# Kernel tuning notes

Hardware: AMD Instinct MI355X
Metric: run time of the kernel (lower is better)

Reference implementation:

```python
import jax, jax.numpy as jnp
import numpy as np

N, C, NUM_SPECIES, D = 2048, 128, 10, 9  # nodes, channels, species, irreps dim (0e+1o+2e)
IR_DIMS = {"0e": 1, "1o": 3, "2e": 5}
MULS = {3: {"0e": 10, "1o": 11, "2e": 13}, 2: {"0e": 3, "1o": 2, "2e": 3}, 1: {"0e": 1, "1o": 1, "2e": 1}}
IRS = ("0e", "1o", "2e")


def setup_inputs() -> dict:
    key = jax.random.key(0)
    ks = iter(jax.random.split(key, 64))
    inp = {}
    inp["node_feats"] = jax.random.normal(next(ks), (N, C, D), dtype=jnp.float32)
    inp["index"] = jax.random.randint(next(ks), (N,), 0, NUM_SPECIES)
    for order in (3, 2, 1):
        for ir in IRS:
            mul, irdim = MULS[order][ir], IR_DIMS[ir]
            u = jax.random.normal(next(ks), (D,) * order + (mul, irdim), dtype=jnp.float32) * 0.1
            mask = jax.random.bernoulli(next(ks), 0.2, u.shape).astype(jnp.float32)
            inp[f"U{order}_{ir}"] = u * mask
            # learnable per-species weights, stddev mul**-0.5 (gradient_normalization='element')
            inp[f"W{order}_{ir}"] = jax.random.normal(next(ks), (NUM_SPECIES, mul, C), dtype=jnp.float32) * (mul ** -0.5)
    return inp


def _forward(x, index, Us, Ws):
    # x: [N, C, D] node features; index: [N] species ids
    out = {}
    for order in (3, 2, 1):
        created = set()
        for ir in IRS:
            u = Us[(order, ir)]                 # (D,)*order + (mul, ir_dim)
            w = Ws[(order, ir)][index]          # [N, mul, C] species-indexed gather
            if ir not in out:
                # first appearance: contract one feature index j and the basis mul k at once
                out[ir] = jnp.einsum('...jki,nkc,ncj->nc...i', u, w, x)
                created.add(ir)
            else:
                out[ir] = out[ir] + jnp.einsum('...ki,nkc->nc...i', u, w)
        for ir in IRS:
            if ir in created:
                continue
            # contract one remaining feature index with x each order
            out[ir] = jnp.einsum('nc...ji,ncj->nc...i', out[ir], x)
    # concat chunks in sorted irreps order (0e, 1o, 2e) -> [N, C, 9]
    return jnp.concatenate([out[ir] for ir in IRS], axis=-1)


def reference(node_feats, index, U3_0e, U3_1o, U3_2e, U2_0e, U2_1o, U2_2e, U1_0e, U1_1o, U1_2e,
              W3_0e, W3_1o, W3_2e, W2_0e, W2_1o, W2_2e, W1_0e, W1_1o, W1_2e):
    Us = {(3, '0e'): U3_0e, (3, '1o'): U3_1o, (3, '2e'): U3_2e,
          (2, '0e'): U2_0e, (2, '1o'): U2_1o, (2, '2e'): U2_2e,
          (1, '0e'): U1_0e, (1, '1o'): U1_1o, (1, '2e'): U1_2e}
    Ws = {(3, '0e'): W3_0e, (3, '1o'): W3_1o, (3, '2e'): W3_2e,
          (2, '0e'): W2_0e, (2, '1o'): W2_1o, (2, '2e'): W2_2e,
          (1, '0e'): W1_0e, (1, '1o'): W1_1o, (1, '2e'): W1_2e}
    return _forward(node_feats, index, Us, Ws)
```

## Files before the change

kernel.cpp:

```cpp
#include <hip/hip_runtime.h>

#define N_NODES 2048
#define C_CH    128
#define N_SPEC  10

#define PAGE2   2048
#define NMONO   219
#define MAIN_F  1752

#define US3_0   0
#define US3_1   1650
#define US3_2   7095
#define US2_0   17820
#define US2_1   17955
#define US2_2   18225
#define US_TOT  18900

#define US_OFF_B  (128 * 1024)
#define CG_OFF_B  (256 * 1024)
#define CG_BYTES  ((size_t)N_SPEC * C_CH * PAGE2 * 4)

__global__ __launch_bounds__(1024) void bucket_kernel(const int* __restrict__ index,
                                                      int* __restrict__ counts,
                                                      int* __restrict__ lists) {
    __shared__ int sc[N_SPEC];
    const int tid = threadIdx.x;
    if (tid < N_SPEC) sc[tid] = 0;
    __syncthreads();
    for (int n = tid; n < N_NODES; n += blockDim.x) {
        int s = index[n];
        int pos = atomicAdd(&sc[s], 1);
        lists[s * N_NODES + pos] = n;
    }
    __syncthreads();
    if (tid < N_SPEC) counts[tid] = sc[tid];
}

struct Params {
    const float* U3[3]; const float* W3[3];
    const float* U2[3]; const float* W2[3];
    const float* U1[3]; const float* W1[3];
};

__global__ __launch_bounds__(256) void usym_kernel(Params p, float* __restrict__ Us) {
    const int t = blockIdx.x * 256 + threadIdx.x;
    if (t >= US_TOT) return;

    bool is3; int mul, ird, r; const float* u;
    if (t < US3_1)       { is3 = true;  mul = 10; ird = 1; r = t;          u = p.U3[0]; }
    else if (t < US3_2)  { is3 = true;  mul = 11; ird = 3; r = t - US3_1;  u = p.U3[1]; }
    else if (t < US2_0)  { is3 = true;  mul = 13; ird = 5; r = t - US3_2;  u = p.U3[2]; }
    else if (t < US2_1)  { is3 = false; mul = 3;  ird = 1; r = t - US2_0;  u = p.U2[0]; }
    else if (t < US2_2)  { is3 = false; mul = 2;  ird = 3; r = t - US2_1;  u = p.U2[1]; }
    else                 { is3 = false; mul = 3;  ird = 5; r = t - US2_2;  u = p.U2[2]; }

    const int mi  = mul * ird;
    const int n   = r / mi;
    const int rem = r - n * mi;

    float acc = 0.f;
    if (is3) {
        int aa = 0, bb = 0, jj = 0, ctr = 0;
        for (int a2 = 0; a2 < 9; ++a2)
            for (int b2 = a2; b2 < 9; ++b2)
                for (int j2 = b2; j2 < 9; ++j2) {
                    if (ctr == n) { aa = a2; bb = b2; jj = j2; }
                    ++ctr;
                }
        int L[6];
        L[0] = (aa * 9 + bb) * 9 + jj; L[1] = (aa * 9 + jj) * 9 + bb;
        L[2] = (bb * 9 + aa) * 9 + jj; L[3] = (bb * 9 + jj) * 9 + aa;
        L[4] = (jj * 9 + aa) * 9 + bb; L[5] = (jj * 9 + bb) * 9 + aa;
        for (int m = 0; m < 6; ++m) {
            bool dup = false;
            for (int mm = 0; mm < m; ++mm) dup = dup || (L[mm] == L[m]);
            if (!dup) acc += u[L[m] * mi + rem];
        }
    } else {
        int aa = 0, bb = 0, ctr = 0;
        for (int a2 = 0; a2 < 9; ++a2)
            for (int b2 = a2; b2 < 9; ++b2) {
                if (ctr == n) { aa = a2; bb = b2; }
                ++ctr;
            }
        acc = u[(aa * 9 + bb) * mi + rem];
        if (aa != bb) acc += u[(bb * 9 + aa) * mi + rem];
    }
    Us[t] = acc;
}

template <int MUL, int IRD, int IOFF, int MOFF>
__device__ inline void coefRegion(const float* __restrict__ src,
                                  const float* __restrict__ W,
                                  int s, int row0, int rows,
                                  float* __restrict__ Cg, float* __restrict__ sU) {
    const int c   = threadIdx.x;
    float wv[MUL];
#pragma unroll
    for (int k = 0; k < MUL; ++k) wv[k] = W[(s * MUL + k) * C_CH + c];

    const int nfl = rows * MUL * IRD;
    const float* sp = src + row0 * MUL * IRD;
    for (int f = c; f < nfl; f += 128) sU[f] = sp[f];
    __syncthreads();

    const size_t pb = (size_t)(s * C_CH + c) * PAGE2;
    for (int rr = 0; rr < rows; ++rr) {
        const int m = MOFF + row0 + rr;
#pragma unroll
        for (int il = 0; il < IRD; ++il) {
            float a = 0.f;
#pragma unroll
            for (int k = 0; k < MUL; ++k)
                a += sU[(rr * MUL + k) * IRD + il] * wv[k];
            const int i = IOFF + il;
            Cg[pb + (i < 8 ? m * 8 + i : MAIN_F + m)] = a;
        }
    }
}

__global__ __launch_bounds__(128) void coef_kernel(Params p, const float* __restrict__ Us,
                                                   float* __restrict__ Cg) {
    __shared__ float sU[1560];
    const int s = blockIdx.x / 30;
    const int t = blockIdx.x % 30;

    if (t < 7) {
        int rel = t, row0 = rel * 24, rows = (rel == 6) ? 21 : 24;
        coefRegion<10, 1, 0, 0>(Us + US3_0, p.W3[0], s, row0, rows, Cg, sU);
    } else if (t < 14) {
        int rel = t - 7, row0 = rel * 24, rows = (rel == 6) ? 21 : 24;
        coefRegion<11, 3, 1, 0>(Us + US3_1, p.W3[1], s, row0, rows, Cg, sU);
    } else if (t < 21) {
        int rel = t - 14, row0 = rel * 24, rows = (rel == 6) ? 21 : 24;
        coefRegion<13, 5, 4, 0>(Us + US3_2, p.W3[2], s, row0, rows, Cg, sU);
    } else if (t < 23) {
        int rel = t - 21, row0 = rel * 24, rows = (rel == 1) ? 21 : 24;
        coefRegion<3, 1, 0, 165>(Us + US2_0, p.W2[0], s, row0, rows, Cg, sU);
    } else if (t < 25) {
        int rel = t - 23, row0 = rel * 24, rows = (rel == 1) ? 21 : 24;
        coefRegion<2, 3, 1, 165>(Us + US2_1, p.W2[1], s, row0, rows, Cg, sU);
    } else if (t < 27) {
        int rel = t - 25, row0 = rel * 24, rows = (rel == 1) ? 21 : 24;
        coefRegion<3, 5, 4, 165>(Us + US2_2, p.W2[2], s, row0, rows, Cg, sU);
    } else if (t == 27) {
        coefRegion<1, 1, 0, 210>(p.U1[0], p.W1[0], s, 0, 9, Cg, sU);
    } else if (t == 28) {
        coefRegion<1, 3, 1, 210>(p.U1[1], p.W1[1], s, 0, 9, Cg, sU);
    } else {
        coefRegion<1, 5, 4, 210>(p.U1[2], p.W1[2], s, 0, 9, Cg, sU);
    }
}

__device__ inline float selx(const float x[9], int a) {
    float r = x[0];
    r = (a == 1) ? x[1] : r; r = (a == 2) ? x[2] : r; r = (a == 3) ? x[3] : r;
    r = (a == 4) ? x[4] : r; r = (a == 5) ? x[5] : r; r = (a == 6) ? x[6] : r;
    r = (a == 7) ? x[7] : r; r = (a == 8) ? x[8] : r;
    return r;
}

__global__ __launch_bounds__(128) void sc_eval_kernel(const float* __restrict__ nf,
                                                      const int* __restrict__ counts,
                                                      const int* __restrict__ lists,
                                                      const float* __restrict__ Cg,
                                                      float* __restrict__ out) {
    __shared__ __align__(16) float sP[PAGE2];
    const int s = blockIdx.x / C_CH;
    const int c = blockIdx.x % C_CH;
    const float* __restrict__ Cp = Cg + (size_t)(s * C_CH + c) * PAGE2;

    {
        const float4* g = (const float4*)Cp;
        float4* l = (float4*)sP;
#pragma unroll
        for (int q = 0; q < 4; ++q) l[threadIdx.x + 128 * q] = g[threadIdx.x + 128 * q];
    }
    __syncthreads();

    const int cnt = counts[s];
    const float4* __restrict__ Cv = (const float4*)sP;
    const float*  __restrict__ Ct = sP + MAIN_F;

    for (int base = 0; base < cnt; base += 256) {
        const int i0 = base + threadIdx.x;
        const int i1 = base + 128 + threadIdx.x;
        const int m0 = (i0 < cnt) ? lists[s * N_NODES + i0] : -1;
        const int m1 = (i1 < cnt) ? lists[s * N_NODES + i1] : -1;

        const float* x0p = nf + ((long)(m0 < 0 ? 0 : m0) * C_CH + c) * 9;
        const float* x1p = nf + ((long)(m1 < 0 ? 0 : m1) * C_CH + c) * 9;
        float x0[9], x1[9];
#pragma unroll
        for (int j = 0; j < 9; ++j) { x0[j] = x0p[j]; x1[j] = x1p[j]; }

        float4 o0a = {0, 0, 0, 0}, o0b = {0, 0, 0, 0};
        float4 o1a = {0, 0, 0, 0}, o1b = {0, 0, 0, 0};
        float o08 = 0.f, o18 = 0.f;

        const float4* p3 = Cv;
        const float*  t3 = Ct;
        const float4* p2 = Cv + 165 * 2;
        const float*  t2 = Ct + 165;

#pragma unroll 1
        for (int a = 0; a < 9; ++a) {
            const float xa0 = selx(x0, a);
            const float xa1 = selx(x1, a);
            {
                const float4 ca = Cv[(210 + a) * 2], cb = Cv[(210 + a) * 2 + 1];
                const float  c8 = Ct[210 + a];
                o0a += ca * xa0; o0b += cb * xa0; o08 += c8 * xa0;
                o1a += ca * xa1; o1b += cb * xa1; o18 += c8 * xa1;
            }
#pragma unroll 1
            for (int b = a; b < 9; ++b) {
                const float xb0 = selx(x0, b) * xa0;
                const float xb1 = selx(x1, b) * xa1;
                {
                    const float4 ca = p2[0], cb = p2[1];
                    const float  c8 = *t2;
                    o0a += ca * xb0; o0b += cb * xb0; o08 += c8 * xb0;
                    o1a += ca * xb1; o1b += cb * xb1; o18 += c8 * xb1;
                    p2 += 2; ++t2;
                }
#pragma unroll 1
                for (int j = b; j < 9; ++j) {
                    const float mn0 = selx(x0, j) * xb0;
                    const float mn1 = selx(x1, j) * xb1;
                    const float4 ca = p3[0], cb = p3[1];
                    const float  c8 = *t3;
                    o0a += ca * mn0; o0b += cb * mn0; o08 += c8 * mn0;
                    o1a += ca * mn1; o1b += cb * mn1; o18 += c8 * mn1;
                    p3 += 2; ++t3;
                }
            }
        }

        if (m0 >= 0) {
            float* op = out + ((long)m0 * C_CH + c) * 9;
            op[0] = o0a.x; op[1] = o0a.y; op[2] = o0a.z; op[3] = o0a.w;
            op[4] = o0b.x; op[5] = o0b.y; op[6] = o0b.z; op[7] = o0b.w;
            op[8] = o08;
        }
        if (m1 >= 0) {
            float* op = out + ((long)m1 * C_CH + c) * 9;
            op[0] = o1a.x; op[1] = o1a.y; op[2] = o1a.z; op[3] = o1a.w;
            op[4] = o1b.x; op[5] = o1b.y; op[6] = o1b.z; op[7] = o1b.w;
            op[8] = o18;
        }
    }
}

template <int NAB, int MUL, int IRD, int IOFF>
__device__ inline void buildC(const float* __restrict__ u, const float* __restrict__ w,
                              int s, int c, float* __restrict__ sMain, float* __restrict__ sB) {
    const int tid = threadIdx.x;
    const float* wp = w + (s * MUL) * C_CH + c;
    for (int e = tid; e < NAB * IRD; e += 128) {
        int abj = e / IRD;
        int il  = e - abj * IRD;
        const float* up = u + (abj * MUL) * IRD + il;
        float acc = 0.f;
#pragma unroll
        for (int k = 0; k < MUL; ++k)
            acc += up[k * IRD] * wp[k * C_CH];
        int i = IOFF + il;
        if (i < 8) sMain[abj * 8 + i] = acc;
        else       sB[abj] = acc;
    }
}

__global__ __launch_bounds__(128) void sc_kernel(const float* __restrict__ nf,
                                                 const int* __restrict__ counts,
                                                 const int* __restrict__ lists,
                                                 Params p,
                                                 float* __restrict__ out) {
    __shared__ __align__(16) float sC3[729 * 8];
    __shared__ float sC3b[729];
    __shared__ __align__(16) float sC2[81 * 8];
    __shared__ float sC2b[81];
    __shared__ __align__(16) float sC1[9 * 8];
    __shared__ float sC1b[9];

    const int s = blockIdx.x % N_SPEC;
    const int c = blockIdx.x / N_SPEC;
    const int tid = threadIdx.x;

    buildC<729, 10, 1, 0>(p.U3[0], p.W3[0], s, c, sC3, sC3b);
    buildC<729, 11, 3, 1>(p.U3[1], p.W3[1], s, c, sC3, sC3b);
    buildC<729, 13, 5, 4>(p.U3[2], p.W3[2], s, c, sC3, sC3b);
    buildC<81, 3, 1, 0>(p.U2[0], p.W2[0], s, c, sC2, sC2b);
    buildC<81, 2, 3, 1>(p.U2[1], p.W2[1], s, c, sC2, sC2b);
    buildC<81, 3, 5, 4>(p.U2[2], p.W2[2], s, c, sC2, sC2b);
    buildC<9, 1, 1, 0>(p.U1[0], p.W1[0], s, c, sC1, sC1b);
    buildC<9, 1, 3, 1>(p.U1[1], p.W1[1], s, c, sC1, sC1b);
    buildC<9, 1, 5, 4>(p.U1[2], p.W1[2], s, c, sC1, sC1b);
    __syncthreads();

    const int cnt = counts[s];
    const float4* C3v = (const float4*)sC3;
    const float4* C2v = (const float4*)sC2;
    const float4* C1v = (const float4*)sC1;

    for (int base = 0; base < cnt; base += 256) {
        const int i0 = base + tid;
        const int i1 = base + 128 + tid;
        const int m0 = (i0 < cnt) ? lists[s * N_NODES + i0] : -1;
        const int m1 = (i1 < cnt) ? lists[s * N_NODES + i1] : -1;

        const float* x0p = nf + ((long)(m0 < 0 ? 0 : m0) * C_CH + c) * 9;
        const float* x1p = nf + ((long)(m1 < 0 ? 0 : m1) * C_CH + c) * 9;
        float x0[9], x1[9];
#pragma unroll
        for (int j = 0; j < 9; ++j) { x0[j] = x0p[j]; x1[j] = x1p[j]; }

        float4 o0a = {0, 0, 0, 0}, o0b = {0, 0, 0, 0};
        float4 o1a = {0, 0, 0, 0}, o1b = {0, 0, 0, 0};
        float o08 = 0.f, o18 = 0.f;

#pragma unroll 1
        for (int a = 0; a < 9; ++a) {
            const float xa0 = selx(x0, a);
            const float xa1 = selx(x1, a);
            const float4 c1a = C1v[a * 2], c1b = C1v[a * 2 + 1];
            const float  c18 = sC1b[a];
            float4 q0a = c1a, q0b = c1b; float q08 = c18;
            float4 q1a = c1a, q1b = c1b; float q18 = c18;
#pragma unroll
            for (int b = 0; b < 9; ++b) {
                const int ab = a * 9 + b;
                const float4 c2a = C2v[ab * 2], c2b = C2v[ab * 2 + 1];
                const float  c28 = sC2b[ab];
                float4 t0a = c2a, t0b = c2b; float t08 = c28;
                float4 t1a = c2a, t1b = c2b; float t18 = c28;
#pragma unroll
                for (int j = 0; j < 9; ++j) {
                    const int abj = ab * 9 + j;
                    const float4 ca = C3v[abj * 2];
                    const float4 cb = C3v[abj * 2 + 1];
                    const float  c8 = sC3b[abj];
                    t0a += ca * x0[j]; t0b += cb * x0[j]; t08 += c8 * x0[j];
                    t1a += ca * x1[j]; t1b += cb * x1[j]; t18 += c8 * x1[j];
                }
                q0a += t0a * x0[b]; q0b += t0b * x0[b]; q08 += t08 * x0[b];
                q1a += t1a * x1[b]; q1b += t1b * x1[b]; q18 += t18 * x1[b];
            }
            o0a += q0a * xa0; o0b += q0b * xa0; o08 += q08 * xa0;
            o1a += q1a * xa1; o1b += q1b * xa1; o18 += q18 * xa1;
        }

        if (m0 >= 0) {
            float* op = out + ((long)m0 * C_CH + c) * 9;
            op[0] = o0a.x; op[1] = o0a.y; op[2] = o0a.z; op[3] = o0a.w;
            op[4] = o0b.x; op[5] = o0b.y; op[6] = o0b.z; op[7] = o0b.w;
            op[8] = o08;
        }
        if (m1 >= 0) {
            float* op = out + ((long)m1 * C_CH + c) * 9;
            op[0] = o1a.x; op[1] = o1a.y; op[2] = o1a.z; op[3] = o1a.w;
            op[4] = o1b.x; op[5] = o1b.y; op[6] = o1b.z; op[7] = o1b.w;
            op[8] = o18;
        }
    }
}

extern "C" void kernel_launch(void* const* d_in, const int* in_sizes, int n_in,
                              void* d_out, int out_size, void* d_ws, size_t ws_size,
                              hipStream_t stream) {
    const float* nf   = (const float*)d_in[0];
    const int* index  = (const int*)d_in[1];

    Params p;
    p.U3[0] = (const float*)d_in[2];  p.W3[0] = (const float*)d_in[3];
    p.U3[1] = (const float*)d_in[4];  p.W3[1] = (const float*)d_in[5];
    p.U3[2] = (const float*)d_in[6];  p.W3[2] = (const float*)d_in[7];
    p.U2[0] = (const float*)d_in[8];  p.W2[0] = (const float*)d_in[9];
    p.U2[1] = (const float*)d_in[10]; p.W2[1] = (const float*)d_in[11];
    p.U2[2] = (const float*)d_in[12]; p.W2[2] = (const float*)d_in[13];
    p.U1[0] = (const float*)d_in[14]; p.W1[0] = (const float*)d_in[15];
    p.U1[1] = (const float*)d_in[16]; p.W1[1] = (const float*)d_in[17];
    p.U1[2] = (const float*)d_in[18]; p.W1[2] = (const float*)d_in[19];

    int* counts = (int*)d_ws;
    int* lists  = (int*)d_ws + 16;

    bucket_kernel<<<1, 1024, 0, stream>>>(index, counts, lists);

    if (ws_size >= (size_t)CG_OFF_B + CG_BYTES) {
        float* Us = (float*)((char*)d_ws + US_OFF_B);
        float* Cg = (float*)((char*)d_ws + CG_OFF_B);
        usym_kernel<<<(US_TOT + 255) / 256, 256, 0, stream>>>(p, Us);
        coef_kernel<<<N_SPEC * 30, 128, 0, stream>>>(p, Us, Cg);
        sc_eval_kernel<<<N_SPEC * C_CH, 128, 0, stream>>>(nf, counts, lists, Cg,
                                                          (float*)d_out);
    } else {
        sc_kernel<<<N_SPEC * C_CH, 128, 0, stream>>>(nf, counts, lists, p,
                                                     (float*)d_out);
    }
}
```

Before: 181.4 us.

## Split coef kernel over channel quarters; eval four nodes per thread with 64-thread blocks

The coefficient kernel now launches four blocks per (species, region), each covering 32 channels. Weights are staged in shared memory and threads are mapped over (row, irrep) elements, so the per-thread serial row loop shrinks. The eval kernel moves to 64-thread blocks (one wavefront) with each thread handling four nodes instead of two, and partially unrolls the inner j loop. This amortizes the shared-memory coefficient reads over more nodes. The cost is higher register pressure, and with roughly 205 nodes per species many lanes stay idle.

After: 181.6 us. No clear change (+0.1%).

```diff
diff --git a/kernel.cpp b/kernel.cpp
--- a/kernel.cpp
+++ b/kernel.cpp
@@ -90,31 +90,36 @@
 }
 
 template <int MUL, int IRD, int IOFF, int MOFF>
-__device__ inline void coefRegion(const float* __restrict__ src,
-                                  const float* __restrict__ W,
-                                  int s, int row0, int rows,
-                                  float* __restrict__ Cg, float* __restrict__ sU) {
-    const int c   = threadIdx.x;
-    float wv[MUL];
-#pragma unroll
-    for (int k = 0; k < MUL; ++k) wv[k] = W[(s * MUL + k) * C_CH + c];
-
+__device__ inline void coefRegion2(const float* __restrict__ src,
+                                   const float* __restrict__ W,
+                                   int s, int row0, int rows, int c0,
+                                   float* __restrict__ Cg,
+                                   float* __restrict__ sU, float* __restrict__ sW) {
+    const int tid = threadIdx.x;
     const int nfl = rows * MUL * IRD;
     const float* sp = src + row0 * MUL * IRD;
-    for (int f = c; f < nfl; f += 128) sU[f] = sp[f];
+    for (int f = tid; f < nfl; f += 128) sU[f] = sp[f];
+    for (int idx = tid; idx < MUL * 32; idx += 128) {
+        const int k = idx >> 5, cc = idx & 31;
+        sW[idx] = W[(s * MUL + k) * C_CH + c0 + cc];
+    }
     __syncthreads();
 
-    const size_t pb = (size_t)(s * C_CH + c) * PAGE2;
-    for (int rr = 0; rr < rows; ++rr) {
+    const int nel = rows * IRD;
+    for (int f = tid; f < nel; f += 128) {
+        const int rr = f / IRD;
+        const int il = f - rr * IRD;
+        float uv[MUL];
+#pragma unroll
+        for (int k = 0; k < MUL; ++k) uv[k] = sU[(rr * MUL + k) * IRD + il];
         const int m = MOFF + row0 + rr;
-#pragma unroll
-        for (int il = 0; il < IRD; ++il) {
-            float a = 0.f;
-#pragma unroll
-            for (int k = 0; k < MUL; ++k)
-                a += sU[(rr * MUL + k) * IRD + il] * wv[k];
-            const int i = IOFF + il;
-            Cg[pb + (i < 8 ? m * 8 + i : MAIN_F + m)] = a;
+        const int i = IOFF + il;
+        const int off = (i < 8) ? (m * 8 + i) : (MAIN_F + m);
+        for (int cc = 0; cc < 32; ++cc) {
+            float acc = 0.f;
+#pragma unroll
+            for (int k = 0; k < MUL; ++k) acc += uv[k] * sW[k * 32 + cc];
+            Cg[(size_t)(s * C_CH + c0 + cc) * PAGE2 + off] = acc;
         }
     }
 }
@@ -122,33 +127,36 @@
 __global__ __launch_bounds__(128) void coef_kernel(Params p, const float* __restrict__ Us,
                                                    float* __restrict__ Cg) {
     __shared__ float sU[1560];
-    const int s = blockIdx.x / 30;
-    const int t = blockIdx.x % 30;
+    __shared__ float sW[13 * 32];
+    const int s   = blockIdx.x / 120;
+    const int rem = blockIdx.x % 120;
+    const int t   = rem / 4;
+    const int c0  = (rem % 4) * 32;
 
     if (t < 7) {
         int rel = t, row0 = rel * 24, rows = (rel == 6) ? 21 : 24;
-        coefRegion<10, 1, 0, 0>(Us + US3_0, p.W3[0], s, row0, rows, Cg, sU);
+        coefRegion2<10, 1, 0, 0>(Us + US3_0, p.W3[0], s, row0, rows, c0, Cg, sU, sW);
     } else if (t < 14) {
         int rel = t - 7, row0 = rel * 24, rows = (rel == 6) ? 21 : 24;
-        coefRegion<11, 3, 1, 0>(Us + US3_1, p.W3[1], s, row0, rows, Cg, sU);
+        coefRegion2<11, 3, 1, 0>(Us + US3_1, p.W3[1], s, row0, rows, c0, Cg, sU, sW);
     } else if (t < 21) {
         int rel = t - 14, row0 = rel * 24, rows = (rel == 6) ? 21 : 24;
-        coefRegion<13, 5, 4, 0>(Us + US3_2, p.W3[2], s, row0, rows, Cg, sU);
+        coefRegion2<13, 5, 4, 0>(Us + US3_2, p.W3[2], s, row0, rows, c0, Cg, sU, sW);
     } else if (t < 23) {
         int rel = t - 21, row0 = rel * 24, rows = (rel == 1) ? 21 : 24;
-        coefRegion<3, 1, 0, 165>(Us + US2_0, p.W2[0], s, row0, rows, Cg, sU);
+        coefRegion2<3, 1, 0, 165>(Us + US2_0, p.W2[0], s, row0, rows, c0, Cg, sU, sW);
     } else if (t < 25) {
         int rel = t - 23, row0 = rel * 24, rows = (rel == 1) ? 21 : 24;
-        coefRegion<2, 3, 1, 165>(Us + US2_1, p.W2[1], s, row0, rows, Cg, sU);
+        coefRegion2<2, 3, 1, 165>(Us + US2_1, p.W2[1], s, row0, rows, c0, Cg, sU, sW);
     } else if (t < 27) {
         int rel = t - 25, row0 = rel * 24, rows = (rel == 1) ? 21 : 24;
-        coefRegion<3, 5, 4, 165>(Us + US2_2, p.W2[2], s, row0, rows, Cg, sU);
+        coefRegion2<3, 5, 4, 165>(Us + US2_2, p.W2[2], s, row0, rows, c0, Cg, sU, sW);
     } else if (t == 27) {
-        coefRegion<1, 1, 0, 210>(p.U1[0], p.W1[0], s, 0, 9, Cg, sU);
+        coefRegion2<1, 1, 0, 210>(p.U1[0], p.W1[0], s, 0, 9, c0, Cg, sU, sW);
     } else if (t == 28) {
-        coefRegion<1, 3, 1, 210>(p.U1[1], p.W1[1], s, 0, 9, Cg, sU);
+        coefRegion2<1, 3, 1, 210>(p.U1[1], p.W1[1], s, 0, 9, c0, Cg, sU, sW);
     } else {
-        coefRegion<1, 5, 4, 210>(p.U1[2], p.W1[2], s, 0, 9, Cg, sU);
+        coefRegion2<1, 5, 4, 210>(p.U1[2], p.W1[2], s, 0, 9, c0, Cg, sU, sW);
     }
 }
 
@@ -160,11 +168,11 @@
     return r;
 }
 
-__global__ __launch_bounds__(128) void sc_eval_kernel(const float* __restrict__ nf,
-                                                      const int* __restrict__ counts,
-                                                      const int* __restrict__ lists,
-                                                      const float* __restrict__ Cg,
-                                                      float* __restrict__ out) {
+__global__ __launch_bounds__(64) void sc_eval_kernel(const float* __restrict__ nf,
+                                                     const int* __restrict__ counts,
+                                                     const int* __restrict__ lists,
+                                                     const float* __restrict__ Cg,
+                                                     float* __restrict__ out) {
     __shared__ __align__(16) float sP[PAGE2];
     const int s = blockIdx.x / C_CH;
     const int c = blockIdx.x % C_CH;
@@ -174,7 +182,7 @@
         const float4* g = (const float4*)Cp;
         float4* l = (float4*)sP;
 #pragma unroll
-        for (int q = 0; q < 4; ++q) l[threadIdx.x + 128 * q] = g[threadIdx.x + 128 * q];
+        for (int q = 0; q < 8; ++q) l[threadIdx.x + 64 * q] = g[threadIdx.x + 64 * q];
     }
     __syncthreads();
 
@@ -183,20 +191,23 @@
     const float*  __restrict__ Ct = sP + MAIN_F;
 
     for (int base = 0; base < cnt; base += 256) {
-        const int i0 = base + threadIdx.x;
-        const int i1 = base + 128 + threadIdx.x;
-        const int m0 = (i0 < cnt) ? lists[s * N_NODES + i0] : -1;
-        const int m1 = (i1 < cnt) ? lists[s * N_NODES + i1] : -1;
-
-        const float* x0p = nf + ((long)(m0 < 0 ? 0 : m0) * C_CH + c) * 9;
-        const float* x1p = nf + ((long)(m1 < 0 ? 0 : m1) * C_CH + c) * 9;
-        float x0[9], x1[9];
-#pragma unroll
-        for (int j = 0; j < 9; ++j) { x0[j] = x0p[j]; x1[j] = x1p[j]; }
-
-        float4 o0a = {0, 0, 0, 0}, o0b = {0, 0, 0, 0};
-        float4 o1a = {0, 0, 0, 0}, o1b = {0, 0, 0, 0};
-        float o08 = 0.f, o18 = 0.f;
+        int mm[4];
+        float x[4][9];
+#pragma unroll
+        for (int u = 0; u < 4; ++u) {
+            const int i = base + threadIdx.x + 64 * u;
+            mm[u] = (i < cnt) ? lists[s * N_NODES + i] : -1;
+            const float* xp = nf + ((long)(mm[u] < 0 ? 0 : mm[u]) * C_CH + c) * 9;
+#pragma unroll
+            for (int j = 0; j < 9; ++j) x[u][j] = xp[j];
+        }
+
+        float4 oA[4], oB[4];
+        float  o8[4];
+#pragma unroll
+        for (int u = 0; u < 4; ++u) {
+            oA[u] = {0, 0, 0, 0}; oB[u] = {0, 0, 0, 0}; o8[u] = 0.f;
+        }
 
         const float4* p3 = Cv;
         const float*  t3 = Ct;
@@ -205,49 +216,53 @@
 
 #pragma unroll 1
         for (int a = 0; a < 9; ++a) {
-            const float xa0 = selx(x0, a);
-            const float xa1 = selx(x1, a);
+            float xa[4];
+#pragma unroll
+            for (int u = 0; u < 4; ++u) xa[u] = selx(x[u], a);
             {
                 const float4 ca = Cv[(210 + a) * 2], cb = Cv[(210 + a) * 2 + 1];
                 const float  c8 = Ct[210 + a];
-                o0a += ca * xa0; o0b += cb * xa0; o08 += c8 * xa0;
-                o1a += ca * xa1; o1b += cb * xa1; o18 += c8 * xa1;
+#pragma unroll
+                for (int u = 0; u < 4; ++u) {
+                    oA[u] += ca * xa[u]; oB[u] += cb * xa[u]; o8[u] += c8 * xa[u];
+                }
             }
 #pragma unroll 1
             for (int b = a; b < 9; ++b) {
-                const float xb0 = selx(x0, b) * xa0;
-                const float xb1 = selx(x1, b) * xa1;
+                float xb[4];
+#pragma unroll
+                for (int u = 0; u < 4; ++u) xb[u] = selx(x[u], b) * xa[u];
                 {
                     const float4 ca = p2[0], cb = p2[1];
                     const float  c8 = *t2;
-                    o0a += ca * xb0; o0b += cb * xb0; o08 += c8 * xb0;
-                    o1a += ca * xb1; o1b += cb * xb1; o18 += c8 * xb1;
                     p2 += 2; ++t2;
+#pragma unroll
+                    for (int u = 0; u < 4; ++u) {
+                        oA[u] += ca * xb[u]; oB[u] += cb * xb[u]; o8[u] += c8 * xb[u];
+                    }
                 }
-#pragma unroll 1
+#pragma unroll 3
                 for (int j = b; j < 9; ++j) {
-                    const float mn0 = selx(x0, j) * xb0;
-                    const float mn1 = selx(x1, j) * xb1;
                     const float4 ca = p3[0], cb = p3[1];
                     const float  c8 = *t3;
-                    o0a += ca * mn0; o0b += cb * mn0; o08 += c8 * mn0;
-                    o1a += ca * mn1; o1b += cb * mn1; o18 += c8 * mn1;
                     p3 += 2; ++t3;
+#pragma unroll
+                    for (int u = 0; u < 4; ++u) {
+                        const float mn = selx(x[u], j) * xb[u];
+                        oA[u] += ca * mn; oB[u] += cb * mn; o8[u] += c8 * mn;
+                    }
                 }
             }
         }
 
-        if (m0 >= 0) {
-            float* op = out + ((long)m0 * C_CH + c) * 9;
-            op[0] = o0a.x; op[1] = o0a.y; op[2] = o0a.z; op[3] = o0a.w;
-            op[4] = o0b.x; op[5] = o0b.y; op[6] = o0b.z; op[7] = o0b.w;
-            op[8] = o08;
-        }
-        if (m1 >= 0) {
-            float* op = out + ((long)m1 * C_CH + c) * 9;
-            op[0] = o1a.x; op[1] = o1a.y; op[2] = o1a.z; op[3] = o1a.w;
-            op[4] = o1b.x; op[5] = o1b.y; op[6] = o1b.z; op[7] = o1b.w;
-            op[8] = o18;
+#pragma unroll
+        for (int u = 0; u < 4; ++u) {
+            if (mm[u] >= 0) {
+                float* op = out + ((long)mm[u] * C_CH + c) * 9;
+                op[0] = oA[u].x; op[1] = oA[u].y; op[2] = oA[u].z; op[3] = oA[u].w;
+                op[4] = oB[u].x; op[5] = oB[u].y; op[6] = oB[u].z; op[7] = oB[u].w;
+                op[8] = o8[u];
+            }
         }
     }
 }
@@ -391,9 +406,9 @@
         float* Us = (float*)((char*)d_ws + US_OFF_B);
         float* Cg = (float*)((char*)d_ws + CG_OFF_B);
         usym_kernel<<<(US_TOT + 255) / 256, 256, 0, stream>>>(p, Us);
-        coef_kernel<<<N_SPEC * 30, 128, 0, stream>>>(p, Us, Cg);
-        sc_eval_kernel<<<N_SPEC * C_CH, 128, 0, stream>>>(nf, counts, lists, Cg,
-                                                          (float*)d_out);
+        coef_kernel<<<N_SPEC * 30 * 4, 128, 0, stream>>>(p, Us, Cg);
+        sc_eval_kernel<<<N_SPEC * C_CH, 64, 0, stream>>>(nf, counts, lists, Cg,
+                                                         (float*)d_out);
     } else {
         sc_kernel<<<N_SPEC * C_CH, 128, 0, stream>>>(nf, counts, lists, p,
                                                      (float*)d_out);
```
